# Optimization experiments

Hardware: AMD Instinct MI355X
Metric: run time of the kernel (lower is better)

The kernel has to match this reference:

```python
import jax, jax.numpy as jnp
import numpy as np

NEG_INF = -1e30  # stand-in for float('-inf'); avoids inf-inf NaN edge cases, same softmax result


def setup_inputs() -> dict:
    key = jax.random.key(0)
    k1, k2, k3, k4, k5 = jax.random.split(key, 5)
    B, T, C, H = 16, 2048, 200, 64
    x = jax.random.normal(k1, (B, T, C), dtype=jnp.float32)
    # padding mask over key positions, broadcastable to [B, T, T]
    padding_mask = jax.random.randint(k2, (B, 1, T), 0, 2, dtype=jnp.int32)
    # nn.Linear(n_embd, head_size, bias=False) weights, stored as [C, H] so y = x @ W
    Wk = jax.random.normal(k3, (C, H), dtype=jnp.float32) * (C ** -0.5)
    Wq = jax.random.normal(k4, (C, H), dtype=jnp.float32) * (C ** -0.5)
    Wv = jax.random.normal(k5, (C, H), dtype=jnp.float32) * (C ** -0.5)
    return {"x": x, "padding_mask": padding_mask, "Wk": Wk, "Wq": Wq, "Wv": Wv}


def reference(x, padding_mask, Wk, Wq, Wv):
    # x: [B,T,C]; padding_mask: [B,1,T] (0 = padded key position)
    k = x @ Wk  # [B,T,H]
    q = x @ Wq  # [B,T,H]
    v = x @ Wv  # [B,T,H]
    scale = k.shape[-1] ** -0.5
    wei = jnp.einsum("bqh,bkh->bqk", q, k) * scale  # [B,T,T]
    # mask padded key columns before softmax
    wei = jnp.where(padding_mask == 0, NEG_INF, wei)
    wei = jax.nn.softmax(wei, axis=-1)
    # mask padded query rows (transpose of padding mask) to exact zero after softmax
    mask_t = jnp.swapaxes(padding_mask, -2, -1)  # [B,T,1]
    wei = jnp.where(mask_t == 0, 0.0, wei)
    # dropout is identity in eval mode
    out = jnp.einsum("bqk,bkh->bqh", wei, v)  # [B,T,H]
    return out
```

## Files before the change

kernel.cpp:

```cpp
#include <hip/hip_runtime.h>


typedef __attribute__((ext_vector_type(8))) __bf16 bf16x8;
typedef __attribute__((ext_vector_type(4))) __bf16 bf16x4;
typedef __attribute__((ext_vector_type(4))) float f32x4;

#define T_SEQ 2048
#define C_DIM 200
#define H_DIM 64
#define BT_TOT 32768
#define QKV_ELEMS 2097152
#define PPAD 72
#define OPAD 68
#define LOG2E 1.44269504088896f

__global__ __launch_bounds__(256) void qkv_proj(const float* __restrict__ Wk,
                                                const float* __restrict__ Wq,
                                                const float* __restrict__ Wv,
                                                const float* __restrict__ x,
                                                __bf16* __restrict__ qb,
                                                __bf16* __restrict__ kb,
                                                __bf16* __restrict__ vT) {
    __shared__ __bf16 Wl[24576];

    const int tid = threadIdx.x;
    const int wave = tid >> 6, lane = tid & 63, l15 = lane & 15, quad = lane >> 4;
    const int m0b = blockIdx.x * 64;
    const int row0 = m0b + wave * 16;

    f32x4 acc[3][4] = {};

    #pragma unroll
    for (int w = 0; w < 3; ++w) {
        const float* W = (w == 0) ? Wq : (w == 1) ? Wk : Wv;
        const float scale = (w == 0) ? 0.125f * LOG2E : 1.f;
        for (int i = tid; i < 8192; i += 256) {
            const int c = i >> 6, h = i & 63;
            const float val = W[i] * scale;
            const int ks = c >> 5, cq = (c >> 3) & 3, j = c & 7;
            const int t = h >> 4, hl = h & 15;
            Wl[((ks * 12 + w * 4 + t) << 9) + (cq * 16 + hl) * 8 + j] = (__bf16)val;
        }
    }
    __syncthreads();
    #pragma unroll
    for (int ks = 0; ks < 4; ++ks) {
        const float* xr = x + (size_t)(row0 + l15) * C_DIM + ks * 32 + quad * 8;
        const float4 f0 = *(const float4*)xr;
        const float4 f1 = *(const float4*)(xr + 4);
        bf16x8 a;
        a[0]=(__bf16)f0.x; a[1]=(__bf16)f0.y; a[2]=(__bf16)f0.z; a[3]=(__bf16)f0.w;
        a[4]=(__bf16)f1.x; a[5]=(__bf16)f1.y; a[6]=(__bf16)f1.z; a[7]=(__bf16)f1.w;
        #pragma unroll
        for (int w = 0; w < 3; ++w)
            #pragma unroll
            for (int t = 0; t < 4; ++t) {
                const bf16x8 bf = *(const bf16x8*)(Wl + ((ks * 12 + w * 4 + t) << 9) + lane * 8);
                acc[w][t] = __builtin_amdgcn_mfma_f32_16x16x32_bf16(a, bf, acc[w][t], 0, 0, 0);
            }
    }
    __syncthreads();

    #pragma unroll
    for (int w = 0; w < 3; ++w) {
        const float* W = (w == 0) ? Wq : (w == 1) ? Wk : Wv;
        const float scale = (w == 0) ? 0.125f * LOG2E : 1.f;
        for (int i = tid; i < 4608; i += 256) {
            const int c = 128 + (i >> 6), h = i & 63;
            const float val = W[c * H_DIM + h] * scale;
            const int t = h >> 4, hl = h & 15;
            int addr;
            if (c < 192) {
                const int ks = c >> 5, cq = (c >> 3) & 3, j = c & 7;
                addr = (((ks - 4) * 12 + w * 4 + t) << 9) + (cq * 16 + hl) * 8 + j;
            } else {
                addr = 12288 + ((w * 4 + t) << 7) + hl * 8 + (c - 192);
            }
            Wl[addr] = (__bf16)val;
        }
    }
    __syncthreads();
    #pragma unroll
    for (int ks = 4; ks < 7; ++ks) {
        bf16x8 a;
        if (ks < 6 || quad == 0) {
            const float* xr = x + (size_t)(row0 + l15) * C_DIM + ks * 32 + quad * 8;
            const float4 f0 = *(const float4*)xr;
            const float4 f1 = *(const float4*)(xr + 4);
            a[0]=(__bf16)f0.x; a[1]=(__bf16)f0.y; a[2]=(__bf16)f0.z; a[3]=(__bf16)f0.w;
            a[4]=(__bf16)f1.x; a[5]=(__bf16)f1.y; a[6]=(__bf16)f1.z; a[7]=(__bf16)f1.w;
        } else {
            #pragma unroll
            for (int j = 0; j < 8; ++j) a[j] = (__bf16)0.f;
        }
        #pragma unroll
        for (int w = 0; w < 3; ++w)
            #pragma unroll
            for (int t = 0; t < 4; ++t) {
                const int off = (ks < 6) ? (((ks - 4) * 12 + w * 4 + t) << 9) + lane * 8
                                         : 12288 + ((w * 4 + t) << 7) + l15 * 8;
                const bf16x8 bf = *(const bf16x8*)(Wl + off);
                acc[w][t] = __builtin_amdgcn_mfma_f32_16x16x32_bf16(a, bf, acc[w][t], 0, 0, 0);
            }
    }

    #pragma unroll
    for (int t = 0; t < 4; ++t)
        #pragma unroll
        for (int r = 0; r < 4; ++r) {
            const size_t m = row0 + quad * 4 + r;
            qb[m * H_DIM + t * 16 + l15] = (__bf16)acc[0][t][r];
            kb[m * H_DIM + t * 16 + l15] = (__bf16)acc[1][t][r];
        }
    __syncthreads();
    #pragma unroll
    for (int t = 0; t < 4; ++t)
        #pragma unroll
        for (int r = 0; r < 4; ++r)
            Wl[(t * 16 + l15) * 72 + wave * 16 + quad * 4 + r] = (__bf16)acc[2][t][r];
    __syncthreads();
    const int bb = m0b >> 11, tloc = m0b & 2047;
    #pragma unroll
    for (int i = 0; i < 2; ++i) {
        const int seg = i * 256 + tid;
        const int h = seg >> 3, s8 = seg & 7;
        *(bf16x8*)(vT + ((size_t)bb * H_DIM + h) * T_SEQ + tloc + s8 * 8) =
            *(const bf16x8*)(Wl + h * 72 + s8 * 8);
    }
}

__global__ __launch_bounds__(256, 1) void attn(const __bf16* __restrict__ qb,
                                               const __bf16* __restrict__ kb,
                                               const __bf16* __restrict__ vT,
                                               const int* __restrict__ pm,
                                               float* __restrict__ out) {
    __shared__ __align__(16) char arena[8192 + 73728];
    float* biasS = (float*)arena;

    const int tid = threadIdx.x;
    const int wave = tid >> 6, lane = tid & 63, l15 = lane & 15, quad = lane >> 4;
    const int ks = wave;
    const int b = blockIdx.y;
    const int q0 = blockIdx.x * 128;
    const size_t bT = (size_t)b * T_SEQ;

    for (int i = tid; i < 512; i += 256) {
        const int4 p4 = *(const int4*)(pm + bT + i * 4);
        biasS[i * 4 + 0] = p4.x ? 0.f : -1e30f;
        biasS[i * 4 + 1] = p4.y ? 0.f : -1e30f;
        biasS[i * 4 + 2] = p4.z ? 0.f : -1e30f;
        biasS[i * 4 + 3] = p4.w ? 0.f : -1e30f;
    }
    __syncthreads();

    bf16x8 qa[8][2];
    #pragma unroll
    for (int mt = 0; mt < 8; ++mt)
        #pragma unroll
        for (int s = 0; s < 2; ++s)
            qa[mt][s] = *(const bf16x8*)(qb + (bT + q0 + mt * 16 + l15) * H_DIM + s * 32 + quad * 8);

    __bf16* P = (__bf16*)(arena + 8192) + wave * (128 * PPAD);
    const __bf16* kbase = kb + bT * H_DIM;
    const __bf16* vbase = vT + (size_t)b * H_DIM * T_SEQ;

    f32x4 oacc[8][4] = {};
    float lsum[8] = {};

    for (int kt = 0; kt < 8; ++kt) {
        const int key0 = ks * 512 + kt * 64;

        #pragma unroll
        for (int n = 0; n < 4; ++n) {
            const f32x4 bias = *(const f32x4*)(biasS + key0 + n * 16 + quad * 4);
            bf16x8 kf[2];
            #pragma unroll
            for (int s = 0; s < 2; ++s)
                kf[s] = *(const bf16x8*)(kbase + (key0 + n * 16 + l15) * H_DIM + s * 32 + quad * 8);
            f32x4 s_[8];
            #pragma unroll
            for (int mt = 0; mt < 8; ++mt) s_[mt] = bias;
            #pragma unroll
            for (int s = 0; s < 2; ++s)
                #pragma unroll
                for (int mt = 0; mt < 8; ++mt)
                    s_[mt] = __builtin_amdgcn_mfma_f32_16x16x32_bf16(kf[s], qa[mt][s], s_[mt], 0, 0, 0);
            #pragma unroll
            for (int mt = 0; mt < 8; ++mt) {
                bf16x4 p4;
                #pragma unroll
                for (int r = 0; r < 4; ++r) {
                    const float e = exp2f(s_[mt][r]);
                    lsum[mt] += e;
                    p4[r] = (__bf16)e;
                }
                *(bf16x4*)(P + (mt * 16 + l15) * PPAD + n * 16 + quad * 4) = p4;
            }
        }

        bf16x8 pa[8][2];
        #pragma unroll
        for (int mt = 0; mt < 8; ++mt)
            #pragma unroll
            for (int s = 0; s < 2; ++s)
                pa[mt][s] = *(const bf16x8*)(P + (mt * 16 + l15) * PPAD + s * 32 + quad * 8);

        #pragma unroll
        for (int t = 0; t < 4; ++t) {
            bf16x8 vf[2];
            #pragma unroll
            for (int s = 0; s < 2; ++s)
                vf[s] = *(const bf16x8*)(vbase + (size_t)(t * 16 + l15) * T_SEQ + key0 + s * 32 + quad * 8);
            #pragma unroll
            for (int s = 0; s < 2; ++s)
                #pragma unroll
                for (int mt = 0; mt < 8; ++mt)
                    oacc[mt][t] = __builtin_amdgcn_mfma_f32_16x16x32_bf16(pa[mt][s], vf[s], oacc[mt][t], 0, 0, 0);
        }
    }

    #pragma unroll
    for (int mt = 0; mt < 8; ++mt) {
        lsum[mt] += __shfl_xor(lsum[mt], 16, 64);
        lsum[mt] += __shfl_xor(lsum[mt], 32, 64);
    }

    float* Ocomb = (float*)(arena + 8192);
    float* Lcomb = Ocomb + 128 * OPAD;

    __syncthreads();
    #pragma unroll
    for (int step = 0; step < 4; ++step) {
        const int who = (step == 3) ? 0 : step + 1;
        if (ks == who) {
            #pragma unroll
            for (int mt = 0; mt < 8; ++mt) {
                if (step == 0) {
                    #pragma unroll
                    for (int t = 0; t < 4; ++t)
                        #pragma unroll
                        for (int r = 0; r < 4; ++r)
                            Ocomb[(mt * 16 + quad * 4 + r) * OPAD + t * 16 + l15] = oacc[mt][t][r];
                    if (quad == 0) Lcomb[mt * 16 + l15] = lsum[mt];
                } else {
                    #pragma unroll
                    for (int t = 0; t < 4; ++t)
                        #pragma unroll
                        for (int r = 0; r < 4; ++r)
                            Ocomb[(mt * 16 + quad * 4 + r) * OPAD + t * 16 + l15] += oacc[mt][t][r];
                    if (quad == 0) Lcomb[mt * 16 + l15] += lsum[mt];
                }
            }
        }
        __syncthreads();
    }

    #pragma unroll
    for (int mi = 0; mi < 2; ++mi) {
        const int mt = ks * 2 + mi;
        #pragma unroll
        for (int r = 0; r < 4; ++r) {
            const int qpos = q0 + mt * 16 + quad * 4 + r;
            const float lv = Lcomb[mt * 16 + quad * 4 + r];
            const bool qvalid = biasS[qpos] == 0.f;
            const float inv = (qvalid && lv > 0.f) ? 1.f / lv : 0.f;
            #pragma unroll
            for (int t = 0; t < 4; ++t)
                out[(bT + qpos) * H_DIM + t * 16 + l15] =
                    Ocomb[(mt * 16 + quad * 4 + r) * OPAD + t * 16 + l15] * inv;
        }
    }
}

extern "C" void kernel_launch(void* const* d_in, const int* in_sizes, int n_in,
                              void* d_out, int out_size, void* d_ws, size_t ws_size,
                              hipStream_t stream) {
    const float* x  = (const float*)d_in[0];
    const int* pm   = (const int*)d_in[1];
    const float* Wk = (const float*)d_in[2];
    const float* Wq = (const float*)d_in[3];
    const float* Wv = (const float*)d_in[4];
    float* out = (float*)d_out;

    __bf16* qb = (__bf16*)d_ws;
    __bf16* kb = qb + QKV_ELEMS;
    __bf16* vT = kb + QKV_ELEMS;

    qkv_proj<<<dim3(BT_TOT / 64), dim3(256), 0, stream>>>(Wk, Wq, Wv, x, qb, kb, vT);
    attn<<<dim3(T_SEQ / 128, 16), dim3(256), 0, stream>>>(qb, kb, vT, pm, out);
}
```

Baseline: 142.8 us.

## Split attention keys over eight waves and pre-pack weights in a separate kernel

The attention kernel now runs 512 threads (eight waves), each covering 256 keys instead of 512. The serial four-step cross-wave reduction is replaced by zeroing shared memory and combining with shared-memory atomicAdd. A new prep_w kernel converts and permutes the projection weights to bf16 once, so each qkv_proj block copies pre-packed weights with vector loads instead of scattering from fp32. Risks are more register pressure under the 512/2 launch bound, atomic contention in shared memory, and an extra kernel launch.

```diff
diff --git a/kernel.cpp b/kernel.cpp
--- a/kernel.cpp
+++ b/kernel.cpp
@@ -12,16 +12,42 @@
 #define QKV_ELEMS 2097152
 #define PPAD 72
 #define OPAD 68
+#define WTF_FULL 36864
+#define WTF_ELEMS 38400
+#define WTF_A_ELEMS 24576
 #define LOG2E 1.44269504088896f
 
-__global__ __launch_bounds__(256) void qkv_proj(const float* __restrict__ Wk,
-                                                const float* __restrict__ Wq,
-                                                const float* __restrict__ Wv,
-                                                const float* __restrict__ x,
+__global__ void prep_w(const float* __restrict__ Wk, const float* __restrict__ Wq,
+                       const float* __restrict__ Wv, __bf16* __restrict__ WtF) {
+    int idx = blockIdx.x * 256 + threadIdx.x;
+    if (idx >= WTF_ELEMS) return;
+    int w, c, h;
+    if (idx < WTF_FULL) {
+        int j = idx & 7, lane = (idx >> 3) & 63;
+        int chunk = idx >> 9;
+        int t = chunk & 3, rest = chunk >> 2;
+        w = rest % 3; int ks = rest / 3;
+        c = ks * 32 + (lane >> 4) * 8 + j;
+        h = t * 16 + (lane & 15);
+    } else {
+        int i2 = idx - WTF_FULL;
+        int j = i2 & 7, l15 = (i2 >> 3) & 15, t = (i2 >> 7) & 3;
+        w = i2 >> 9;
+        c = 192 + j;
+        h = t * 16 + l15;
+    }
+    const float* W = (w == 0) ? Wq : (w == 1) ? Wk : Wv;
+    float val = W[c * H_DIM + h];
+    if (w == 0) val *= 0.125f * LOG2E;
+    WtF[idx] = (__bf16)val;
+}
+
+__global__ __launch_bounds__(256) void qkv_proj(const float* __restrict__ x,
+                                                const __bf16* __restrict__ WtF,
                                                 __bf16* __restrict__ qb,
                                                 __bf16* __restrict__ kb,
                                                 __bf16* __restrict__ vT) {
-    __shared__ __bf16 Wl[24576];
+    __shared__ __bf16 Wl[WTF_A_ELEMS];
 
     const int tid = threadIdx.x;
     const int wave = tid >> 6, lane = tid & 63, l15 = lane & 15, quad = lane >> 4;
@@ -31,16 +57,9 @@
     f32x4 acc[3][4] = {};
 
     #pragma unroll
-    for (int w = 0; w < 3; ++w) {
-        const float* W = (w == 0) ? Wq : (w == 1) ? Wk : Wv;
-        const float scale = (w == 0) ? 0.125f * LOG2E : 1.f;
-        for (int i = tid; i < 8192; i += 256) {
-            const int c = i >> 6, h = i & 63;
-            const float val = W[i] * scale;
-            const int ks = c >> 5, cq = (c >> 3) & 3, j = c & 7;
-            const int t = h >> 4, hl = h & 15;
-            Wl[((ks * 12 + w * 4 + t) << 9) + (cq * 16 + hl) * 8 + j] = (__bf16)val;
-        }
+    for (int i = 0; i < 12; ++i) {
+        const int c = i * 256 + tid;
+        *(bf16x8*)(Wl + c * 8) = *(const bf16x8*)(WtF + c * 8);
     }
     __syncthreads();
     #pragma unroll
@@ -62,22 +81,10 @@
     __syncthreads();
 
     #pragma unroll
-    for (int w = 0; w < 3; ++w) {
-        const float* W = (w == 0) ? Wq : (w == 1) ? Wk : Wv;
-        const float scale = (w == 0) ? 0.125f * LOG2E : 1.f;
-        for (int i = tid; i < 4608; i += 256) {
-            const int c = 128 + (i >> 6), h = i & 63;
-            const float val = W[c * H_DIM + h] * scale;
-            const int t = h >> 4, hl = h & 15;
-            int addr;
-            if (c < 192) {
-                const int ks = c >> 5, cq = (c >> 3) & 3, j = c & 7;
-                addr = (((ks - 4) * 12 + w * 4 + t) << 9) + (cq * 16 + hl) * 8 + j;
-            } else {
-                addr = 12288 + ((w * 4 + t) << 7) + hl * 8 + (c - 192);
-            }
-            Wl[addr] = (__bf16)val;
-        }
+    for (int i = 0; i < 7; ++i) {
+        const int c = i * 256 + tid;
+        if (c < 1728)
+            *(bf16x8*)(Wl + c * 8) = *(const bf16x8*)(WtF + WTF_A_ELEMS + c * 8);
     }
     __syncthreads();
     #pragma unroll
@@ -129,12 +136,12 @@
     }
 }
 
-__global__ __launch_bounds__(256, 1) void attn(const __bf16* __restrict__ qb,
+__global__ __launch_bounds__(512, 2) void attn(const __bf16* __restrict__ qb,
                                                const __bf16* __restrict__ kb,
                                                const __bf16* __restrict__ vT,
                                                const int* __restrict__ pm,
                                                float* __restrict__ out) {
-    __shared__ __align__(16) char arena[8192 + 73728];
+    __shared__ __align__(16) char arena[8192 + 8 * 128 * PPAD * 2];
     float* biasS = (float*)arena;
 
     const int tid = threadIdx.x;
@@ -144,12 +151,12 @@
     const int q0 = blockIdx.x * 128;
     const size_t bT = (size_t)b * T_SEQ;
 
-    for (int i = tid; i < 512; i += 256) {
-        const int4 p4 = *(const int4*)(pm + bT + i * 4);
-        biasS[i * 4 + 0] = p4.x ? 0.f : -1e30f;
-        biasS[i * 4 + 1] = p4.y ? 0.f : -1e30f;
-        biasS[i * 4 + 2] = p4.z ? 0.f : -1e30f;
-        biasS[i * 4 + 3] = p4.w ? 0.f : -1e30f;
+    {
+        const int4 p4 = *(const int4*)(pm + bT + tid * 4);
+        biasS[tid * 4 + 0] = p4.x ? 0.f : -1e30f;
+        biasS[tid * 4 + 1] = p4.y ? 0.f : -1e30f;
+        biasS[tid * 4 + 2] = p4.z ? 0.f : -1e30f;
+        biasS[tid * 4 + 3] = p4.w ? 0.f : -1e30f;
     }
     __syncthreads();
 
@@ -167,8 +174,8 @@
     f32x4 oacc[8][4] = {};
     float lsum[8] = {};
 
-    for (int kt = 0; kt < 8; ++kt) {
-        const int key0 = ks * 512 + kt * 64;
+    for (int kt = 0; kt < 4; ++kt) {
+        const int key0 = ks * 256 + kt * 64;
 
         #pragma unroll
         for (int n = 0; n < 4; ++n) {
@@ -229,35 +236,29 @@
     float* Lcomb = Ocomb + 128 * OPAD;
 
     __syncthreads();
-    #pragma unroll
-    for (int step = 0; step < 4; ++step) {
-        const int who = (step == 3) ? 0 : step + 1;
-        if (ks == who) {
-            #pragma unroll
-            for (int mt = 0; mt < 8; ++mt) {
-                if (step == 0) {
-                    #pragma unroll
-                    for (int t = 0; t < 4; ++t)
-                        #pragma unroll
-                        for (int r = 0; r < 4; ++r)
-                            Ocomb[(mt * 16 + quad * 4 + r) * OPAD + t * 16 + l15] = oacc[mt][t][r];
-                    if (quad == 0) Lcomb[mt * 16 + l15] = lsum[mt];
-                } else {
-                    #pragma unroll
-                    for (int t = 0; t < 4; ++t)
-                        #pragma unroll
-                        for (int r = 0; r < 4; ++r)
-                            Ocomb[(mt * 16 + quad * 4 + r) * OPAD + t * 16 + l15] += oacc[mt][t][r];
-                    if (quad == 0) Lcomb[mt * 16 + l15] += lsum[mt];
-                }
-            }
-        }
-        __syncthreads();
-    }
-
-    #pragma unroll
-    for (int mi = 0; mi < 2; ++mi) {
-        const int mt = ks * 2 + mi;
+    {
+        f32x4* Z = (f32x4*)Ocomb;
+        const f32x4 zv = {0.f, 0.f, 0.f, 0.f};
+        #pragma unroll
+        for (int i = 0; i < 5; ++i) {
+            const int idx = i * 512 + tid;
+            if (idx < 2208) Z[idx] = zv;
+        }
+    }
+    __syncthreads();
+    #pragma unroll
+    for (int mt = 0; mt < 8; ++mt) {
+        #pragma unroll
+        for (int t = 0; t < 4; ++t)
+            #pragma unroll
+            for (int r = 0; r < 4; ++r)
+                atomicAdd(&Ocomb[(mt * 16 + quad * 4 + r) * OPAD + t * 16 + l15], oacc[mt][t][r]);
+        if (quad == 0) atomicAdd(&Lcomb[mt * 16 + l15], lsum[mt]);
+    }
+    __syncthreads();
+
+    {
+        const int mt = wave;
         #pragma unroll
         for (int r = 0; r < 4; ++r) {
             const int qpos = q0 + mt * 16 + quad * 4 + r;
@@ -282,10 +283,12 @@
     const float* Wv = (const float*)d_in[4];
     float* out = (float*)d_out;
 
-    __bf16* qb = (__bf16*)d_ws;
-    __bf16* kb = qb + QKV_ELEMS;
-    __bf16* vT = kb + QKV_ELEMS;
-
-    qkv_proj<<<dim3(BT_TOT / 64), dim3(256), 0, stream>>>(Wk, Wq, Wv, x, qb, kb, vT);
-    attn<<<dim3(T_SEQ / 128, 16), dim3(256), 0, stream>>>(qb, kb, vT, pm, out);
-}
+    __bf16* qb  = (__bf16*)d_ws;
+    __bf16* kb  = qb + QKV_ELEMS;
+    __bf16* vT  = kb + QKV_ELEMS;
+    __bf16* WtF = vT + QKV_ELEMS;
+
+    prep_w<<<dim3((WTF_ELEMS + 255) / 256), dim3(256), 0, stream>>>(Wk, Wq, Wv, WtF);
+    qkv_proj<<<dim3(BT_TOT / 64), dim3(256), 0, stream>>>(x, WtF, qb, kb, vT);
+    attn<<<dim3(T_SEQ / 128, 16), dim3(512), 0, stream>>>(qb, kb, vT, pm, out);
+}
```

Measured after the change: 238.9 us. 1.67x slower.
